# Optimization experiments

Hardware: AMD Instinct MI355X
Metric: run time of the kernel (lower is better)

The kernel has to match this reference:

```python
import jax, jax.numpy as jnp
import numpy as np

N_NODES = 50000
N_EDGES = 800000
IN_CH = 128
HIDDEN = 256
OUT_DIM = 1
N_GRAPHS = 64


def setup_inputs() -> dict:
    key = jax.random.key(0)
    ks = jax.random.split(key, 9)
    x = jax.random.normal(ks[0], (N_NODES, IN_CH), dtype=jnp.float32)
    edge_index = jax.random.randint(ks[1], (2, N_EDGES), 0, N_NODES)
    batch = jnp.sort(jax.random.randint(ks[2], (N_NODES,), 0, N_GRAPHS))
    # GCNConv weight (lin has no bias; bias added after aggregation in PyG)
    w1 = jax.random.normal(ks[3], (IN_CH, HIDDEN), dtype=jnp.float32) * 0.05
    b1 = jnp.zeros((HIDDEN,), dtype=jnp.float32)
    # FFNN head
    w2 = jax.random.normal(ks[4], (HIDDEN, HIDDEN), dtype=jnp.float32) * 0.05
    b2 = jnp.zeros((HIDDEN,), dtype=jnp.float32)
    w3 = jax.random.normal(ks[5], (HIDDEN, OUT_DIM), dtype=jnp.float32) * 0.05
    b3 = jnp.zeros((OUT_DIM,), dtype=jnp.float32)
    return {"x": x, "edge_index": edge_index, "batch": batch,
            "w1": w1, "b1": b1, "w2": w2, "b2": b2, "w3": w3, "b3": b3}


def reference(x, edge_index, batch, w1, b1, w2, b2, w3, b3):
    N = x.shape[0]
    # --- GCNConv: symmetric-normalized aggregation with self-loops ---
    loop = jnp.arange(N)
    src = jnp.concatenate([edge_index[0], loop])  # [E+N]
    dst = jnp.concatenate([edge_index[1], loop])  # [E+N]
    h = x @ w1  # transform first (in_ch -> hidden), PyG order
    deg = jax.ops.segment_sum(jnp.ones_like(dst, dtype=h.dtype), dst, num_segments=N)
    deg_inv_sqrt = jnp.where(deg > 0, jax.lax.rsqrt(deg), 0.0)
    norm = deg_inv_sqrt[src] * deg_inv_sqrt[dst]  # [E+N]
    msg = h[src] * norm[:, None]  # [E+N, hidden]
    h = jax.ops.segment_sum(msg, dst, num_segments=N) + b1  # [N, hidden]
    h = jax.nn.relu(h)
    # --- global_mean_pool over batch ids ---
    cnt = jax.ops.segment_sum(jnp.ones((N,), dtype=h.dtype), batch, num_segments=N_GRAPHS)
    pooled = jax.ops.segment_sum(h, batch, num_segments=N_GRAPHS)
    pooled = pooled / jnp.maximum(cnt, 1.0)[:, None]  # [G, hidden]
    # --- FFNN head (dropout is identity in eval mode) ---
    z = jax.nn.relu(pooled @ w2 + b2)
    return z @ w3 + b3  # [G, out_dim]
```

## Files before the change

### kernel.cpp

```cpp
#include <hip/hip_runtime.h>

#define IN_CH   128
#define HIDDEN  256
#define N_GRAPHS 64
#define GN 64

typedef short short8 __attribute__((ext_vector_type(8)));
typedef float f32x4 __attribute__((ext_vector_type(4)));

__device__ inline unsigned f2bf(float f) {
  unsigned u = __float_as_uint(f);
  return (u + 0x7fffu + ((u >> 16) & 1u)) >> 16;
}
__device__ inline unsigned pack2(float lo, float hi) {
  return (f2bf(hi) << 16) | f2bf(lo);
}
__device__ inline void acc8(uint4 v, float w, float* A) {
  A[0] += w * __uint_as_float(v.x << 16);
  A[1] += w * __uint_as_float(v.x & 0xffff0000u);
  A[2] += w * __uint_as_float(v.y << 16);
  A[3] += w * __uint_as_float(v.y & 0xffff0000u);
  A[4] += w * __uint_as_float(v.z << 16);
  A[5] += w * __uint_as_float(v.z & 0xffff0000u);
  A[6] += w * __uint_as_float(v.w << 16);
  A[7] += w * __uint_as_float(v.w & 0xffff0000u);
}

__global__ void k_pre(const float* __restrict__ x, ushort* __restrict__ xh,
                      const float* __restrict__ w1, ushort* __restrict__ w1t,
                      const int* __restrict__ dst, int* __restrict__ deg,
                      int* __restrict__ rank, int total8, int e) {
  int i = blockIdx.x * blockDim.x + threadIdx.x;
  if (i < total8) {
    const float4* xp = reinterpret_cast<const float4*>(x) + (size_t)i * 2;
    float4 a = xp[0], b = xp[1];
    uint4 o;
    o.x = pack2(a.x, a.y);
    o.y = pack2(a.z, a.w);
    o.z = pack2(b.x, b.y);
    o.w = pack2(b.z, b.w);
    reinterpret_cast<uint4*>(xh)[i] = o;
  }
  if (i < HIDDEN * IN_CH) {
    int nn = i >> 7, k = i & 127;
    w1t[i] = (ushort)f2bf(w1[k * 256 + nn]);
  }
  if (i < e) {
    rank[i] = atomicAdd(&deg[dst[i]], 1);
  }
}

__global__ __launch_bounds__(1024) void k_scan1(const int* __restrict__ deg,
    int* __restrict__ offs, int* __restrict__ bsum, int n) {
  __shared__ int sm[1024];
  int t = threadIdx.x;
  int i = blockIdx.x * 1024 + t;
  int v = (i < n) ? deg[i] : 0;
  sm[t] = v;
  __syncthreads();
  for (int d = 1; d < 1024; d <<= 1) {
    int add = (t >= d) ? sm[t - d] : 0;
    __syncthreads();
    sm[t] += add;
    __syncthreads();
  }
  if (i < n) offs[i] = sm[t] - v;
  if (t == 1023) bsum[blockIdx.x] = sm[1023];
}

__global__ void k_scan23(int* __restrict__ offs, const int* __restrict__ bsum,
                         const int* __restrict__ deg, float* __restrict__ dinv,
                         int n, int nb) {
  __shared__ int bofs_s[64];
  int t = threadIdx.x;
  if (t < 64) {
    int orig = (t < nb) ? bsum[t] : 0;
    int v = orig;
    for (int d = 1; d < 64; d <<= 1) {
      int u = __shfl_up(v, d, 64);
      if (t >= d) v += u;
    }
    bofs_s[t] = v - orig;
  }
  __syncthreads();
  int i = blockIdx.x * blockDim.x + t;
  if (i < n) {
    offs[i] += bofs_s[i >> 10];
    dinv[i] = 1.0f / sqrtf((float)(deg[i] + 1));
  }
}

__global__ void k_place(const int* __restrict__ src, const int* __restrict__ dst,
                        const int* __restrict__ rank, const int* __restrict__ offs,
                        int* __restrict__ csr, int e) {
  int i = blockIdx.x * blockDim.x + threadIdx.x;
  if (i < e) csr[offs[dst[i]] + rank[i]] = src[i];
}

__global__ __launch_bounds__(256) void k_agg(const ushort* __restrict__ xh,
    const int* __restrict__ csr, const int* __restrict__ offs,
    const int* __restrict__ degc, const float* __restrict__ dinv,
    ushort* __restrict__ yh, int n) {
  int node = blockIdx.x * 4 + (threadIdx.x >> 6);
  if (node >= n) return;
  int lane = threadIdx.x & 63;
  int es = lane >> 4;
  int cg = lane & 15;
  int o = offs[node], c = degc[node];
  float A[8] = {0.f, 0.f, 0.f, 0.f, 0.f, 0.f, 0.f, 0.f};
  for (int it = 0; it < c; it += 16) {
    float w[4];
    uint4 v[4];
#pragma unroll
    for (int u = 0; u < 4; ++u) {
      int ii = it + u * 4 + es;
      bool val = ii < c;
      int s = val ? csr[o + ii] : node;
      w[u] = val ? dinv[s] : 0.f;
      v[u] = *reinterpret_cast<const uint4*>(&xh[(size_t)s * IN_CH + cg * 8]);
    }
#pragma unroll
    for (int u = 0; u < 4; ++u) acc8(v[u], w[u], A);
  }
#pragma unroll
  for (int k = 0; k < 8; ++k) {
    A[k] += __shfl_xor(A[k], 16, 64);
    A[k] += __shfl_xor(A[k], 32, 64);
  }
  if (es == 0) {
    float dn = dinv[node];
    uint4 xs = *reinterpret_cast<const uint4*>(&xh[(size_t)node * IN_CH + cg * 8]);
    float xv[8] = {0.f, 0.f, 0.f, 0.f, 0.f, 0.f, 0.f, 0.f};
    acc8(xs, dn, xv);
    float v[8];
#pragma unroll
    for (int k = 0; k < 8; ++k) v[k] = (A[k] + xv[k]) * dn;
    uint4 w;
    w.x = pack2(v[0], v[1]);
    w.y = pack2(v[2], v[3]);
    w.z = pack2(v[4], v[5]);
    w.w = pack2(v[6], v[7]);
    *reinterpret_cast<uint4*>(&yh[(size_t)node * IN_CH + cg * 8]) = w;
  }
}

__global__ __launch_bounds__(256) void k_gemmpool(
    const ushort* __restrict__ yh, const ushort* __restrict__ w1t,
    const float* __restrict__ b1, const int* __restrict__ batch,
    float* __restrict__ pooled, int n) {
  __shared__ float part[4][HIDDEN];
  __shared__ int bl[GN];
  int t = threadIdx.x;
  int node0 = blockIdx.x * GN;

  if (t < GN) {
    int nd = node0 + t;
    bl[t] = (nd < n) ? batch[nd] : -1;
  }
  {
    float* pp = &part[0][0];
    for (int i = t; i < 4 * HIDDEN; i += 256) pp[i] = 0.f;
  }

  int wv = t >> 6, l = t & 63;
  int lr = l & 15;
  int lk = l >> 4;
  int colbase = wv * 64;

  f32x4 acc[4][4];
#pragma unroll
  for (int m = 0; m < 4; ++m)
#pragma unroll
    for (int nn = 0; nn < 4; ++nn) acc[m][nn] = (f32x4){0.f, 0.f, 0.f, 0.f};

#pragma unroll
  for (int kc = 0; kc < 4; ++kc) {
    short8 a[4], b[4];
#pragma unroll
    for (int m = 0; m < 4; ++m)
      a[m] = *reinterpret_cast<const short8*>(
          &yh[(size_t)(node0 + m * 16 + lr) * IN_CH + kc * 32 + lk * 8]);
#pragma unroll
    for (int nn = 0; nn < 4; ++nn)
      b[nn] = *reinterpret_cast<const short8*>(
          &w1t[(size_t)(colbase + nn * 16 + lr) * IN_CH + kc * 32 + lk * 8]);
#pragma unroll
    for (int m = 0; m < 4; ++m)
#pragma unroll
      for (int nn = 0; nn < 4; ++nn)
        acc[m][nn] = __builtin_amdgcn_mfma_f32_16x16x32_bf16(a[m], b[nn], acc[m][nn], 0, 0, 0);
  }

  __syncthreads();

  float bias[4];
#pragma unroll
  for (int nn = 0; nn < 4; ++nn) bias[nn] = b1[colbase + nn * 16 + lr];
  int g0 = bl[0];

#pragma unroll
  for (int m = 0; m < 4; ++m) {
    float s[4] = {0.f, 0.f, 0.f, 0.f};
    int gcur = -1;
#pragma unroll
    for (int j = 0; j < 4; ++j) {
      int row = m * 16 + lk * 4 + j;
      int node = node0 + row;
      int g = (node < n) ? bl[row] : -1;
      if (g != gcur) {
        if (gcur >= 0) {
          int gi = gcur - g0;
          if (gi < 4) {
#pragma unroll
            for (int nn = 0; nn < 4; ++nn)
              atomicAdd(&part[gi][colbase + nn * 16 + lr], s[nn]);
          } else {
#pragma unroll
            for (int nn = 0; nn < 4; ++nn)
              atomicAdd(&pooled[gcur * HIDDEN + colbase + nn * 16 + lr], s[nn]);
          }
        }
#pragma unroll
        for (int u = 0; u < 4; ++u) s[u] = 0.f;
        gcur = g;
      }
      if (g >= 0) {
#pragma unroll
        for (int nn = 0; nn < 4; ++nn)
          s[nn] += fmaxf(acc[m][nn][j] + bias[nn], 0.f);
      }
    }
    if (gcur >= 0) {
      int gi = gcur - g0;
      if (gi < 4) {
#pragma unroll
        for (int nn = 0; nn < 4; ++nn)
          atomicAdd(&part[gi][colbase + nn * 16 + lr], s[nn]);
      } else {
#pragma unroll
        for (int nn = 0; nn < 4; ++nn)
          atomicAdd(&pooled[gcur * HIDDEN + colbase + nn * 16 + lr], s[nn]);
      }
    }
  }

  __syncthreads();
  int lastIdx = min(GN, n - node0) - 1;
  int gmax = bl[lastIdx];
  int span = gmax - g0;
  if (span > 3) span = 3;
  for (int gi = 0; gi <= span; ++gi) {
    atomicAdd(&pooled[(g0 + gi) * HIDDEN + t], part[gi][t]);
  }
}

__global__ __launch_bounds__(256) void k_head(const float* __restrict__ pooled,
    const int* __restrict__ batch, int n, const float* __restrict__ w2,
    const float* __restrict__ b2, const float* __restrict__ w3,
    const float* __restrict__ b3, float* __restrict__ out) {
  __shared__ float p[256];
  __shared__ float red[4];
  __shared__ int scnt;
  int g = blockIdx.x, t = threadIdx.x;
  if (t == 0) {
    int lo = 0, hi = n;
    while (lo < hi) { int mid = (lo + hi) >> 1; if (batch[mid] < g) lo = mid + 1; else hi = mid; }
    int a = lo;
    lo = 0; hi = n;
    int g1 = g + 1;
    while (lo < hi) { int mid = (lo + hi) >> 1; if (batch[mid] < g1) lo = mid + 1; else hi = mid; }
    scnt = lo - a;
  }
  __syncthreads();
  float c = (float)max(scnt, 1);
  p[t] = pooled[g * HIDDEN + t] / c;
  __syncthreads();
  float a = 0.f;
  for (int k = 0; k < 256; ++k) a += p[k] * w2[k * 256 + t];
  a += b2[t];
  a = fmaxf(a, 0.f);
  float part = a * w3[t];
  for (int off = 32; off > 0; off >>= 1) part += __shfl_down(part, off, 64);
  if ((t & 63) == 0) red[t >> 6] = part;
  __syncthreads();
  if (t == 0) out[g] = red[0] + red[1] + red[2] + red[3] + b3[0];
}

extern "C" void kernel_launch(void* const* d_in, const int* in_sizes, int n_in,
                              void* d_out, int out_size, void* d_ws, size_t ws_size,
                              hipStream_t stream) {
  const float* x    = (const float*)d_in[0];
  const int*   ei   = (const int*)d_in[1];
  const int*   batch= (const int*)d_in[2];
  const float* w1   = (const float*)d_in[3];
  const float* b1   = (const float*)d_in[4];
  const float* w2   = (const float*)d_in[5];
  const float* b2   = (const float*)d_in[6];
  const float* w3   = (const float*)d_in[7];
  const float* b3   = (const float*)d_in[8];
  float* out = (float*)d_out;

  int N = in_sizes[2];
  int E = in_sizes[1] / 2;
  const int* esrc = ei;
  const int* edst = ei + E;
  int NP = ((N + 63) / 64) * 64;
  (void)NP;

  int* W = (int*)d_ws;
  int*    deg_i  = W;
  float*  pooled = (float*)(W + N);
  int*    offs   = W + N + N_GRAPHS * HIDDEN;
  float*  dinv   = (float*)(offs + N);
  int*    bsum   = (int*)(dinv + N);
  int*    rank   = bsum + 64;
  int*    csr    = rank + E;
  ushort* w1t    = (ushort*)(csr + E);
  ushort* xh     = (ushort*)(csr + E + 16384);
  ushort* yh     = xh + (size_t)N * IN_CH;

  hipMemsetAsync(deg_i, 0, (size_t)(N + N_GRAPHS * HIDDEN) * sizeof(int), stream);

  const int tb = 256;
  int total8 = N * 16;
  int preN = max(total8, E);
  k_pre<<<(preN + tb - 1) / tb, tb, 0, stream>>>(x, xh, w1, w1t, edst, deg_i, rank, total8, E);
  int nb = (N + 1023) / 1024;
  k_scan1<<<nb, 1024, 0, stream>>>(deg_i, offs, bsum, N);
  k_scan23<<<(N + tb - 1) / tb, tb, 0, stream>>>(offs, bsum, deg_i, dinv, N, nb);
  k_place<<<(E + tb - 1) / tb, tb, 0, stream>>>(esrc, edst, rank, offs, csr, E);
  k_agg<<<(N + 3) / 4, 256, 0, stream>>>(xh, csr, offs, deg_i, dinv, yh, N);
  k_gemmpool<<<(N + GN - 1) / GN, 256, 0, stream>>>(yh, w1t, b1, batch, pooled, N);
  k_head<<<N_GRAPHS, 256, 0, stream>>>(pooled, batch, N, w2, b2, w3, b3, out);
}
```

Measured before the change: 153.9 us.

## Replace global-atomic CSR build with two-level bucketed counting sort

Replaces the per-edge global atomic degree count, three-kernel scan and scattered placement with a two-level counting sort. Edges are first bucketed by destination/128 using shared-memory histograms and a per-bucket scan, then each bucket block sorts its edges into the CSR and computes offsets, degrees and dinv locally. The aim is to remove contended global atomics and random global scatters. In exchange it adds kernel launches, an intermediate edge buffer written and read again, and a single-block scan; the CSR order within a node becomes nondeterministic.

```diff
diff --git a/kernel.cpp b/kernel.cpp
--- a/kernel.cpp
+++ b/kernel.cpp
@@ -4,6 +4,9 @@
 #define HIDDEN  256
 #define N_GRAPHS 64
 #define GN 64
+#define NPB 128
+#define MAXBUCK 512
+#define NBLK 400
 
 typedef short short8 __attribute__((ext_vector_type(8)));
 typedef float f32x4 __attribute__((ext_vector_type(4)));
@@ -26,75 +29,124 @@
   A[7] += w * __uint_as_float(v.w & 0xffff0000u);
 }
 
-__global__ void k_pre(const float* __restrict__ x, ushort* __restrict__ xh,
-                      const float* __restrict__ w1, ushort* __restrict__ w1t,
-                      const int* __restrict__ dst, int* __restrict__ deg,
-                      int* __restrict__ rank, int total8, int e) {
-  int i = blockIdx.x * blockDim.x + threadIdx.x;
-  if (i < total8) {
+__global__ __launch_bounds__(256) void k_p1(
+    const float* __restrict__ x, ushort* __restrict__ xh,
+    const float* __restrict__ w1, ushort* __restrict__ w1t,
+    const int* __restrict__ dst, int* __restrict__ ghist,
+    int total8, int e, int nbuck, int chunk) {
+  __shared__ int h[MAXBUCK];
+  int t = threadIdx.x, b = blockIdx.x;
+  for (int k = t; k < nbuck; k += 256) h[k] = 0;
+  int gid = b * 256 + t;
+  const int nthr = NBLK * 256;
+  for (int i = gid; i < total8; i += nthr) {
     const float4* xp = reinterpret_cast<const float4*>(x) + (size_t)i * 2;
-    float4 a = xp[0], b = xp[1];
+    float4 a = xp[0], bb = xp[1];
     uint4 o;
     o.x = pack2(a.x, a.y);
     o.y = pack2(a.z, a.w);
-    o.z = pack2(b.x, b.y);
-    o.w = pack2(b.z, b.w);
+    o.z = pack2(bb.x, bb.y);
+    o.w = pack2(bb.z, bb.w);
     reinterpret_cast<uint4*>(xh)[i] = o;
   }
-  if (i < HIDDEN * IN_CH) {
-    int nn = i >> 7, k = i & 127;
-    w1t[i] = (ushort)f2bf(w1[k * 256 + nn]);
-  }
-  if (i < e) {
-    rank[i] = atomicAdd(&deg[dst[i]], 1);
-  }
-}
-
-__global__ __launch_bounds__(1024) void k_scan1(const int* __restrict__ deg,
-    int* __restrict__ offs, int* __restrict__ bsum, int n) {
-  __shared__ int sm[1024];
+  if (gid < HIDDEN * IN_CH) {
+    int nn = gid >> 7, k = gid & 127;
+    w1t[gid] = (ushort)f2bf(w1[k * 256 + nn]);
+  }
+  __syncthreads();
+  int s = b * chunk, eend = min(e, s + chunk);
+  for (int i = s + t; i < eend; i += 256) atomicAdd(&h[dst[i] >> 7], 1);
+  __syncthreads();
+  for (int k = t; k < nbuck; k += 256) ghist[b * MAXBUCK + k] = h[k];
+}
+
+__global__ __launch_bounds__(512) void k_p2a(const int* __restrict__ ghist,
+    int* __restrict__ boff, int* __restrict__ total, int nbuck) {
+  __shared__ int sm[512];
+  int k = blockIdx.x, t = threadIdx.x;
+  int v = (t < NBLK) ? ghist[t * MAXBUCK + k] : 0;
+  sm[t] = v;
+  __syncthreads();
+  for (int d = 1; d < 512; d <<= 1) {
+    int add = (t >= d) ? sm[t - d] : 0;
+    __syncthreads();
+    sm[t] += add;
+    __syncthreads();
+  }
+  if (t < NBLK) boff[k * NBLK + t] = sm[t] - v;
+  if (t == 511) total[k] = sm[511];
+}
+
+__global__ __launch_bounds__(512) void k_p2b(const int* __restrict__ total,
+    int* __restrict__ tbase, int nbuck) {
+  __shared__ int sm[512];
   int t = threadIdx.x;
-  int i = blockIdx.x * 1024 + t;
-  int v = (i < n) ? deg[i] : 0;
+  int v = (t < nbuck) ? total[t] : 0;
   sm[t] = v;
   __syncthreads();
-  for (int d = 1; d < 1024; d <<= 1) {
+  for (int d = 1; d < 512; d <<= 1) {
     int add = (t >= d) ? sm[t - d] : 0;
     __syncthreads();
     sm[t] += add;
     __syncthreads();
   }
-  if (i < n) offs[i] = sm[t] - v;
-  if (t == 1023) bsum[blockIdx.x] = sm[1023];
-}
-
-__global__ void k_scan23(int* __restrict__ offs, const int* __restrict__ bsum,
-                         const int* __restrict__ deg, float* __restrict__ dinv,
-                         int n, int nb) {
-  __shared__ int bofs_s[64];
-  int t = threadIdx.x;
-  if (t < 64) {
-    int orig = (t < nb) ? bsum[t] : 0;
-    int v = orig;
-    for (int d = 1; d < 64; d <<= 1) {
-      int u = __shfl_up(v, d, 64);
-      if (t >= d) v += u;
+  if (t < nbuck) tbase[t] = sm[t] - v;
+}
+
+__global__ __launch_bounds__(256) void k_p3(
+    const int* __restrict__ src, const int* __restrict__ dst,
+    const int* __restrict__ boff, const int* __restrict__ tbase,
+    int2* __restrict__ ebuf, int e, int nbuck, int chunk) {
+  __shared__ int cur[MAXBUCK];
+  int t = threadIdx.x, b = blockIdx.x;
+  for (int k = t; k < nbuck; k += 256) cur[k] = tbase[k] + boff[k * NBLK + b];
+  __syncthreads();
+  int s = b * chunk, eend = min(e, s + chunk);
+  for (int i = s + t; i < eend; i += 256) {
+    int d = dst[i];
+    int pos = atomicAdd(&cur[d >> 7], 1);
+    ebuf[pos] = make_int2(src[i], d);
+  }
+}
+
+__global__ __launch_bounds__(256) void k_p4(const int2* __restrict__ ebuf,
+    const int* __restrict__ tbase, int* __restrict__ csr, int* __restrict__ offs,
+    int* __restrict__ deg, float* __restrict__ dinv, int n, int nbuck, int etot) {
+  __shared__ int dcnt[NPB];
+  __shared__ int doff[NPB];
+  __shared__ int dcur[NPB];
+  int k = blockIdx.x, t = threadIdx.x;
+  int s = tbase[k];
+  int eend = (k + 1 < nbuck) ? tbase[k + 1] : etot;
+  if (t < NPB) dcnt[t] = 0;
+  __syncthreads();
+  for (int i = s + t; i < eend; i += 256) atomicAdd(&dcnt[ebuf[i].y & (NPB - 1)], 1);
+  __syncthreads();
+  if (t < NPB) doff[t] = dcnt[t];
+  __syncthreads();
+  for (int d = 1; d < NPB; d <<= 1) {
+    int add = 0;
+    if (t < NPB && t >= d) add = doff[t - d];
+    __syncthreads();
+    if (t < NPB) doff[t] += add;
+    __syncthreads();
+  }
+  if (t < NPB) {
+    int ex = doff[t] - dcnt[t];
+    dcur[t] = s + ex;
+    int node = k * NPB + t;
+    if (node < n) {
+      offs[node] = s + ex;
+      deg[node] = dcnt[t];
+      dinv[node] = 1.0f / sqrtf((float)(dcnt[t] + 1));
     }
-    bofs_s[t] = v - orig;
-  }
-  __syncthreads();
-  int i = blockIdx.x * blockDim.x + t;
-  if (i < n) {
-    offs[i] += bofs_s[i >> 10];
-    dinv[i] = 1.0f / sqrtf((float)(deg[i] + 1));
-  }
-}
-
-__global__ void k_place(const int* __restrict__ src, const int* __restrict__ dst,
-                        const int* __restrict__ rank, const int* __restrict__ offs,
-                        int* __restrict__ csr, int e) {
-  int i = blockIdx.x * blockDim.x + threadIdx.x;
-  if (i < e) csr[offs[dst[i]] + rank[i]] = src[i];
+  }
+  __syncthreads();
+  for (int i = s + t; i < eend; i += 256) {
+    int2 ed = ebuf[i];
+    int pos = atomicAdd(&dcur[ed.y & (NPB - 1)], 1);
+    csr[pos] = ed.x;
+  }
 }
 
 __global__ __launch_bounds__(256) void k_agg(const ushort* __restrict__ xh,
@@ -304,31 +356,33 @@
   int E = in_sizes[1] / 2;
   const int* esrc = ei;
   const int* edst = ei + E;
-  int NP = ((N + 63) / 64) * 64;
-  (void)NP;
+  int nbuck = (N + NPB - 1) / NPB;
+  int chunk = (E + NBLK - 1) / NBLK;
 
   int* W = (int*)d_ws;
-  int*    deg_i  = W;
-  float*  pooled = (float*)(W + N);
-  int*    offs   = W + N + N_GRAPHS * HIDDEN;
-  float*  dinv   = (float*)(offs + N);
-  int*    bsum   = (int*)(dinv + N);
-  int*    rank   = bsum + 64;
-  int*    csr    = rank + E;
+  int2*   ebuf   = (int2*)W;
+  int*    base1  = W + (size_t)E * 2;
+  float*  pooled = (float*)base1;
+  int*    offs   = base1 + N_GRAPHS * HIDDEN;
+  int*    deg_i  = offs + N;
+  float*  dinv   = (float*)(deg_i + N);
+  int*    total  = (int*)(dinv + N);
+  int*    tbase  = total + MAXBUCK;
+  int*    ghist  = tbase + MAXBUCK;
+  int*    boff   = ghist + NBLK * MAXBUCK;
+  int*    csr    = boff + MAXBUCK * NBLK;
   ushort* w1t    = (ushort*)(csr + E);
   ushort* xh     = (ushort*)(csr + E + 16384);
   ushort* yh     = xh + (size_t)N * IN_CH;
 
-  hipMemsetAsync(deg_i, 0, (size_t)(N + N_GRAPHS * HIDDEN) * sizeof(int), stream);
-
-  const int tb = 256;
+  hipMemsetAsync(pooled, 0, (size_t)(N_GRAPHS * HIDDEN) * sizeof(float), stream);
+
   int total8 = N * 16;
-  int preN = max(total8, E);
-  k_pre<<<(preN + tb - 1) / tb, tb, 0, stream>>>(x, xh, w1, w1t, edst, deg_i, rank, total8, E);
-  int nb = (N + 1023) / 1024;
-  k_scan1<<<nb, 1024, 0, stream>>>(deg_i, offs, bsum, N);
-  k_scan23<<<(N + tb - 1) / tb, tb, 0, stream>>>(offs, bsum, deg_i, dinv, N, nb);
-  k_place<<<(E + tb - 1) / tb, tb, 0, stream>>>(esrc, edst, rank, offs, csr, E);
+  k_p1<<<NBLK, 256, 0, stream>>>(x, xh, w1, w1t, edst, ghist, total8, E, nbuck, chunk);
+  k_p2a<<<nbuck, 512, 0, stream>>>(ghist, boff, total, nbuck);
+  k_p2b<<<1, 512, 0, stream>>>(total, tbase, nbuck);
+  k_p3<<<NBLK, 256, 0, stream>>>(esrc, edst, boff, tbase, ebuf, E, nbuck, chunk);
+  k_p4<<<nbuck, 256, 0, stream>>>(ebuf, tbase, csr, offs, deg_i, dinv, N, nbuck, E);
   k_agg<<<(N + 3) / 4, 256, 0, stream>>>(xh, csr, offs, deg_i, dinv, yh, N);
   k_gemmpool<<<(N + GN - 1) / GN, 256, 0, stream>>>(yh, w1t, b1, batch, pooled, N);
   k_head<<<N_GRAPHS, 256, 0, stream>>>(pooled, batch, N, w2, b2, w3, b3, out);
```

After: 130.8 us. 15.0% less time.
